# Optimization experiments

Measured on AMD Instinct MI355X. Metric: run time of the kernel, lower is better.

## Reference

```python
import jax, jax.numpy as jnp
import numpy as np

N_NODES = 256  # num_eeg_channels; reshape in head forces node count == channels

def setup_inputs() -> dict:
    key = jax.random.key(0)
    ks = jax.random.split(key, 16)
    T, H, L, E = 30000, 512, 256, 32768
    def w(k, shape):
        return jax.random.normal(k, shape, jnp.float32) / np.sqrt(shape[0]).astype(np.float32)
    return {
        "eeg_nodes": jax.random.normal(ks[0], (N_NODES, T), jnp.float32),
        "eeg_idx": jax.random.randint(ks[1], (2, E), 0, N_NODES),
        "eeg_attr": jax.random.uniform(ks[2], (E,), jnp.float32),
        # struct_featurizer GIN: conv1 MLP [T,H,H], conv2 MLP [H,L,L]
        "Ws1a": w(ks[3], (T, H)), "bs1a": jnp.zeros((H,), jnp.float32),
        "Ws1b": w(ks[4], (H, H)), "bs1b": jnp.zeros((H,), jnp.float32),
        "Ws2a": w(ks[5], (H, L)), "bs2a": jnp.zeros((L,), jnp.float32),
        "Ws2b": w(ks[6], (L, L)), "bs2b": jnp.zeros((L,), jnp.float32),
        # gin_scorer GIN: conv1 MLP [L,H,H], conv2 MLP [H,1,1]
        "Wc1a": w(ks[7], (L, H)), "bc1a": jnp.zeros((H,), jnp.float32),
        "Wc1b": w(ks[8], (H, H)), "bc1b": jnp.zeros((H,), jnp.float32),
        "Wc2a": w(ks[9], (H, 1)), "bc2a": jnp.zeros((1,), jnp.float32),
        "Wc2b": w(ks[10], (1, 1)), "bc2b": jnp.zeros((1,), jnp.float32),
        # dementia head: Linear(N*L, 1)
        "Wd": w(ks[11], (N_NODES * L, 1)), "bd": jnp.zeros((1,), jnp.float32),
    }


def _gin_conv(x, src, dst, W1, b1, W2, b2):
    # GINConv, eps=0: nn(x + sum_{j in N(i)} x_j); edge weights unsupported/ignored.
    agg = jax.ops.segment_sum(x[src], dst, num_segments=N_NODES)
    h = x + agg
    h = jax.nn.relu(h @ W1 + b1)  # MLP([in, out, out]) = Linear-ReLU-Linear
    return h @ W2 + b2


def reference(eeg_nodes, eeg_idx, eeg_attr,
              Ws1a, bs1a, Ws1b, bs1b, Ws2a, bs2a, Ws2b, bs2b,
              Wc1a, bc1a, Wc1b, bc1b, Wc2a, bc2a, Wc2b, bc2b,
              Wd, bd):
    src, dst = eeg_idx[0], eeg_idx[1]
    # struct_featurizer (2-layer GIN; inter-layer ReLU, edge_weight ignored by GINConv)
    h = _gin_conv(eeg_nodes, src, dst, Ws1a, bs1a, Ws1b, bs1b)
    h = jax.nn.relu(h)
    feat = _gin_conv(h, src, dst, Ws2a, bs2a, Ws2b, bs2b)  # [N, L]
    # gin_scorer (2-layer GIN)
    s = _gin_conv(feat, src, dst, Wc1a, bc1a, Wc1b, bc1b)
    s = jax.nn.relu(s)
    s = _gin_conv(s, src, dst, Wc2a, bc2a, Wc2b, bc2b)  # [N, 1]
    region_scores = jax.nn.sigmoid(s)
    flat = feat.reshape(1, -1)  # [1, N*L]
    dementia_pred = jax.nn.sigmoid(flat @ Wd + bd)  # [1, 1]
    return dementia_pred, region_scores
```

## Files before the change

### kernel.cpp

```cpp
#include <hip/hip_runtime.h>
#include <math.h>

#define N_NODES 256
#define T_DIM   30000
#define KP      30016
#define H_DIM   512
#define L_DIM   256

typedef __attribute__((ext_vector_type(8))) short short8;
typedef __attribute__((ext_vector_type(4))) float floatx4;

__device__ __forceinline__ unsigned short f2b(float f) {
    unsigned u = __float_as_uint(f);
    u += 0x7fffu + ((u >> 16) & 1u);
    return (unsigned short)(u >> 16);
}

__device__ __forceinline__ float4 zero4() {
    float4 z; z.x = z.y = z.z = z.w = 0.f; return z;
}

__global__ __launch_bounds__(256)
void k_prep(const float* __restrict__ W, const float* __restrict__ x,
            unsigned short* __restrict__ Wt, unsigned short* __restrict__ xb,
            float* __restrict__ P, float* __restrict__ dem,
            float* __restrict__ u) {
    __shared__ float tile[64][65];
    const int b = blockIdx.x, t = threadIdx.x;
    if (b < 3752) {
        const int k0 = (b % 469) << 6;
        const int c0 = (b / 469) << 6;
        const int rr = t >> 4, c4 = (t & 15) << 2;
        #pragma unroll
        for (int i = 0; i < 4; ++i) {
            const int k = k0 + rr + (i << 4);
            float4 v = (k < T_DIM)
                           ? *(const float4*)&W[(size_t)k * H_DIM + c0 + c4]
                           : zero4();
            tile[rr + (i << 4)][c4 + 0] = v.x;
            tile[rr + (i << 4)][c4 + 1] = v.y;
            tile[rr + (i << 4)][c4 + 2] = v.z;
            tile[rr + (i << 4)][c4 + 3] = v.w;
        }
        __syncthreads();
        const int cr = t >> 4, k4 = (t & 15) << 2;
        #pragma unroll
        for (int i = 0; i < 4; ++i) {
            const int c = cr + (i << 4);
            ushort4 o;
            o.x = f2b(tile[k4 + 0][c]);
            o.y = f2b(tile[k4 + 1][c]);
            o.z = f2b(tile[k4 + 2][c]);
            o.w = f2b(tile[k4 + 3][c]);
            *(ushort4*)&Wt[(size_t)(c0 + c) * KP + k0 + k4] = o;
        }
    } else if (b < 7504) {
        const int e0 = (b - 3752) * 2048 + t * 8;
        const int row = e0 / KP;
        const int col = e0 % KP;
        short8 o;
        if (col < T_DIM) {
            float4 v0 = *(const float4*)&x[(size_t)row * T_DIM + col];
            float4 v1 = *(const float4*)&x[(size_t)row * T_DIM + col + 4];
            o[0] = (short)f2b(v0.x); o[1] = (short)f2b(v0.y);
            o[2] = (short)f2b(v0.z); o[3] = (short)f2b(v0.w);
            o[4] = (short)f2b(v1.x); o[5] = (short)f2b(v1.y);
            o[6] = (short)f2b(v1.z); o[7] = (short)f2b(v1.w);
        } else {
            o = (short8){0, 0, 0, 0, 0, 0, 0, 0};
        }
        *(short8*)&xb[e0] = o;
    } else if (b < 7568) {
        const int i0 = ((b - 7504) << 10) + (t << 2);
        float4 v;
        v.x = ((i0 + 0) >> 8) == ((i0 + 0) & 255) ? 1.f : 0.f;
        v.y = ((i0 + 1) >> 8) == ((i0 + 1) & 255) ? 1.f : 0.f;
        v.z = ((i0 + 2) >> 8) == ((i0 + 2) & 255) ? 1.f : 0.f;
        v.w = ((i0 + 3) >> 8) == ((i0 + 3) & 255) ? 1.f : 0.f;
        *(float4*)&P[i0] = v;
    } else {
        if (t < 256) u[t] = 0.f;
        if (t == 0) *dem = 0.f;
    }
}

__global__ void k_init_P(float* P, float* dem, float* u) {
    int t = blockIdx.x * blockDim.x + threadIdx.x;
    P[t] = ((t >> 8) == (t & 255)) ? 1.0f : 0.0f;
    if (t == 0) *dem = 0.0f;
    if (t < 256) u[t] = 0.0f;
}

__global__ void k_count_edges(const int* __restrict__ idx, int E, float* P) {
    int e = blockIdx.x * blockDim.x + threadIdx.x;
    if (e < E) {
        int s = idx[e];
        int d = idx[E + e];
        atomicAdd(&P[d * N_NODES + s], 1.0f);
    }
}

__global__ void k_zero(float* p, int n) {
    int t = blockIdx.x * blockDim.x + threadIdx.x;
    if (t < n) p[t] = 0.0f;
}

__global__ __launch_bounds__(256)
void k_reduce(const float4* __restrict__ Y1p, float4* __restrict__ Y1, int nz,
              const int* __restrict__ idx, int E, float* __restrict__ P) {
    const int b = blockIdx.x, t = threadIdx.x;
    if (b < 128) {
        const int i = (b << 8) | t;
        float4 s = Y1p[i];
        #pragma unroll 4
        for (int z = 1; z < nz; ++z) {
            float4 v = Y1p[(size_t)z * 32768 + i];
            s.x += v.x; s.y += v.y; s.z += v.z; s.w += v.w;
        }
        Y1[i] = s;
    } else {
        const int e = ((b - 128) << 8) + t;
        if (e < E) {
            int s = idx[e];
            int d = idx[E + e];
            atomicAdd(&P[d * N_NODES + s], 1.0f);
        }
    }
}

__global__ __launch_bounds__(256)
void k_gemm_bf16(const unsigned short* __restrict__ xb,
                 const unsigned short* __restrict__ Wt,
                 float* __restrict__ outp, int kc) {
    __shared__ __align__(16) unsigned short Al[128 * 64];
    __shared__ __align__(16) unsigned short Bl[128 * 64];

    const int t = threadIdx.x;
    const int orig = blockIdx.x;
    const int q = gridDim.x >> 3;
    const int L = (orig & 7) * q + (orig >> 3);
    const int tile = L & 7;
    const int colBase = (tile & 3) << 7;
    const int rowBase = (tile >> 2) << 7;
    const int z = L >> 3;
    const int kb0 = z * kc;
    const int kend = min(kb0 + kc, KP);
    const int nchunk = (kend - kb0) >> 6;

    const int sr = t >> 1, sg = (t & 1) << 2;
    const int br = t >> 3, bhc = t & 7;
    const unsigned short* axp = xb + (size_t)(rowBase + sr) * KP + sg * 8;
    const unsigned short* bwp = Wt + (size_t)(colBase + br) * KP + bhc * 8;

    const int w    = t >> 6;
    const int wr   = (w >> 1) << 6;
    const int wc   = (w & 1) << 6;
    const int lane = t & 63;
    const int lm   = lane & 15;
    const int lq   = (lane >> 4) << 3;

    floatx4 acc[4][4];
    #pragma unroll
    for (int i = 0; i < 4; ++i)
        #pragma unroll
        for (int j = 0; j < 4; ++j)
            acc[i][j] = (floatx4){0.f, 0.f, 0.f, 0.f};

    short8 pa[4], pb[4];

#define GLOAD(C) do {                                                          \
        const int kg_ = kb0 + (C) * 64;                                        \
        _Pragma("unroll")                                                      \
        for (int i_ = 0; i_ < 4; ++i_)                                         \
            pa[i_] = *(const short8*)(axp + kg_ + i_ * 8);                     \
        _Pragma("unroll")                                                      \
        for (int i_ = 0; i_ < 4; ++i_)                                         \
            pb[i_] = *(const short8*)(bwp + (size_t)(32 * i_) * KP + kg_);     \
    } while (0)

    GLOAD(0);

    #pragma unroll 1
    for (int c = 0; c < nchunk; ++c) {
        __syncthreads();
        #pragma unroll
        for (int i = 0; i < 4; ++i) {
            const int ga = (sg + i) ^ (sr & 7);
            *(short8*)&Al[sr * 64 + ga * 8] = pa[i];
        }
        #pragma unroll
        for (int i = 0; i < 4; ++i) {
            const int row = br + 32 * i;
            const int gb  = bhc ^ (row & 7);
            *(short8*)&Bl[row * 64 + gb * 8] = pb[i];
        }
        __syncthreads();

        if (c + 1 < nchunk) GLOAD(c + 1);

        #pragma unroll
        for (int s = 0; s < 2; ++s) {
            const int gbase = (s << 2) | (lq >> 3);
            short8 af[4], bf[4];
            #pragma unroll
            for (int i = 0; i < 4; ++i) {
                const int R = wr + i * 16 + lm;
                af[i] = *(const short8*)&Al[R * 64 + ((gbase ^ (R & 7)) << 3)];
            }
            #pragma unroll
            for (int j = 0; j < 4; ++j) {
                const int Cc = wc + j * 16 + lm;
                bf[j] = *(const short8*)&Bl[Cc * 64 + ((gbase ^ (Cc & 7)) << 3)];
            }
            #pragma unroll
            for (int i = 0; i < 4; ++i)
                #pragma unroll
                for (int j = 0; j < 4; ++j)
                    acc[i][j] = __builtin_amdgcn_mfma_f32_16x16x32_bf16(
                        af[i], bf[j], acc[i][j], 0, 0, 0);
        }
    }
#undef GLOAD

    float* op = outp + (size_t)z * (N_NODES * H_DIM);
    const int rq = (lane >> 4) << 2;
    #pragma unroll
    for (int i = 0; i < 4; ++i) {
        #pragma unroll
        for (int j = 0; j < 4; ++j) {
            const int r  = rowBase + wr + i * 16 + rq;
            const int cc = colBase + wc + j * 16 + lm;
            op[(size_t)(r + 0) * H_DIM + cc] = acc[i][j][0];
            op[(size_t)(r + 1) * H_DIM + cc] = acc[i][j][1];
            op[(size_t)(r + 2) * H_DIM + cc] = acc[i][j][2];
            op[(size_t)(r + 3) * H_DIM + cc] = acc[i][j][3];
        }
    }
}

__global__ __launch_bounds__(256)
void k_gemm_big_atomic(const float* __restrict__ x, const float* __restrict__ W,
                       float* __restrict__ outp, int kc) {
    __shared__ float xs[16 * 140];
    __shared__ float ws[16 * 132];
    const int t  = threadIdx.x;
    const int colBase = blockIdx.x * 128;
    const int rowBase = blockIdx.y * 128;
    const int kb0  = blockIdx.z * kc;
    const int kend = min(kb0 + kc, T_DIM);
    const int nchunk = (kend > kb0) ? ((kend - kb0) >> 4) : 0;
    const int lr  = t >> 2, lkq = (t & 3) * 4;
    const int wkk = t >> 5, wcq = (t & 31) * 4;
    const int tx  = t & 15, ty = t >> 4;
    float acc[8][8];
    #pragma unroll
    for (int i = 0; i < 8; ++i)
        #pragma unroll
        for (int j = 0; j < 8; ++j) acc[i][j] = 0.0f;
    #pragma unroll 1
    for (int c = 0; c < nchunk; ++c) {
        int kb = kb0 + c * 16;
        __syncthreads();
        const float* xp = x + (size_t)(rowBase + lr) * T_DIM + kb + lkq;
        float4 xa = *(const float4*)xp;
        float4 xb4 = *(const float4*)(xp + (size_t)64 * T_DIM);
        const float* wp = W + (size_t)(kb + wkk) * H_DIM + colBase + wcq;
        float4 wa = *(const float4*)wp;
        float4 wb = *(const float4*)(wp + 8 * H_DIM);
        xs[(lkq + 0) * 140 + lr] = xa.x; xs[(lkq + 1) * 140 + lr] = xa.y;
        xs[(lkq + 2) * 140 + lr] = xa.z; xs[(lkq + 3) * 140 + lr] = xa.w;
        xs[(lkq + 0) * 140 + lr + 64] = xb4.x; xs[(lkq + 1) * 140 + lr + 64] = xb4.y;
        xs[(lkq + 2) * 140 + lr + 64] = xb4.z; xs[(lkq + 3) * 140 + lr + 64] = xb4.w;
        *(float4*)&ws[wkk * 132 + wcq]       = wa;
        *(float4*)&ws[(wkk + 8) * 132 + wcq] = wb;
        __syncthreads();
        #pragma unroll
        for (int kk = 0; kk < 16; ++kk) {
            float a[8], b[8];
            *(float4*)&a[0] = *(const float4*)&xs[kk * 140 + ty * 8];
            *(float4*)&a[4] = *(const float4*)&xs[kk * 140 + ty * 8 + 4];
            *(float4*)&b[0] = *(const float4*)&ws[kk * 132 + tx * 8];
            *(float4*)&b[4] = *(const float4*)&ws[kk * 132 + tx * 8 + 4];
            #pragma unroll
            for (int i = 0; i < 8; ++i)
                #pragma unroll
                for (int j = 0; j < 8; ++j)
                    acc[i][j] = fmaf(a[i], b[j], acc[i][j]);
        }
    }
    if (nchunk == 0) return;
    #pragma unroll
    for (int i = 0; i < 8; ++i) {
        int r = rowBase + ty * 8 + i;
        #pragma unroll
        for (int j = 0; j < 8; ++j)
            atomicAdd(&outp[r * H_DIM + colBase + tx * 8 + j], acc[i][j]);
    }
}

template<int K, int N, int MODE>
__global__ __launch_bounds__(64)
void k_mstage(const float* __restrict__ A, const float* __restrict__ B,
              const float* __restrict__ bias, float* __restrict__ out, int act,
              const float* __restrict__ Wd, float* __restrict__ dem,
              const float* __restrict__ uW, float* __restrict__ u) {
    const int lane = threadIdx.x;
    const int wv = blockIdx.x;
    const int nct = N >> 4;
    const int r0 = (wv / nct) << 4;
    const int c0 = (wv % nct) << 4;
    const int lm   = lane & 15;
    const int lq   = (lane >> 4) << 3;

    floatx4 accE = {0.f, 0.f, 0.f, 0.f};
    floatx4 accO = {0.f, 0.f, 0.f, 0.f};
    const float* ap = A + (size_t)(r0 + lm) * K + lq;
    const float* bp = B + (size_t)lq * N + c0 + lm;

    #pragma unroll 2
    for (int kb = 0; kb < K; kb += 64) {
        {
            float4 a0 = *(const float4*)(ap + kb);
            float4 a1 = *(const float4*)(ap + kb + 4);
            const float* bq = bp + (size_t)kb * N;
            float b0 = bq[0],           b1 = bq[(size_t)N];
            float b2 = bq[(size_t)2*N], b3 = bq[(size_t)3*N];
            float b4 = bq[(size_t)4*N], b5 = bq[(size_t)5*N];
            float b6 = bq[(size_t)6*N], b7 = bq[(size_t)7*N];
            short8 af, bf;
            af[0] = (short)f2b(a0.x); af[1] = (short)f2b(a0.y);
            af[2] = (short)f2b(a0.z); af[3] = (short)f2b(a0.w);
            af[4] = (short)f2b(a1.x); af[5] = (short)f2b(a1.y);
            af[6] = (short)f2b(a1.z); af[7] = (short)f2b(a1.w);
            bf[0] = (short)f2b(b0); bf[1] = (short)f2b(b1);
            bf[2] = (short)f2b(b2); bf[3] = (short)f2b(b3);
            bf[4] = (short)f2b(b4); bf[5] = (short)f2b(b5);
            bf[6] = (short)f2b(b6); bf[7] = (short)f2b(b7);
            accE = __builtin_amdgcn_mfma_f32_16x16x32_bf16(af, bf, accE, 0, 0, 0);
        }
        {
            const int k2 = kb + 32;
            float4 a0 = *(const float4*)(ap + k2);
            float4 a1 = *(const float4*)(ap + k2 + 4);
            const float* bq = bp + (size_t)k2 * N;
            float b0 = bq[0],           b1 = bq[(size_t)N];
            float b2 = bq[(size_t)2*N], b3 = bq[(size_t)3*N];
            float b4 = bq[(size_t)4*N], b5 = bq[(size_t)5*N];
            float b6 = bq[(size_t)6*N], b7 = bq[(size_t)7*N];
            short8 af, bf;
            af[0] = (short)f2b(a0.x); af[1] = (short)f2b(a0.y);
            af[2] = (short)f2b(a0.z); af[3] = (short)f2b(a0.w);
            af[4] = (short)f2b(a1.x); af[5] = (short)f2b(a1.y);
            af[6] = (short)f2b(a1.z); af[7] = (short)f2b(a1.w);
            bf[0] = (short)f2b(b0); bf[1] = (short)f2b(b1);
            bf[2] = (short)f2b(b2); bf[3] = (short)f2b(b3);
            bf[4] = (short)f2b(b4); bf[5] = (short)f2b(b5);
            bf[6] = (short)f2b(b6); bf[7] = (short)f2b(b7);
            accO = __builtin_amdgcn_mfma_f32_16x16x32_bf16(af, bf, accO, 0, 0, 0);
        }
    }

    const float bb = bias ? bias[c0 + lm] : 0.f;
    const int rq = (lane >> 4) << 2;
    float v[4];
    #pragma unroll
    for (int i = 0; i < 4; ++i) {
        v[i] = accE[i] + accO[i] + bb;
        if (act) v[i] = fmaxf(v[i], 0.f);
    }

    if (MODE == 2) {
        const float uw = uW[c0 + lm];
        #pragma unroll
        for (int i = 0; i < 4; ++i) {
            float p = v[i] * uw;
            #pragma unroll
            for (int off = 8; off; off >>= 1) p += __shfl_down(p, off, 16);
            if (lm == 0) atomicAdd(&u[r0 + rq + i], p);
        }
        return;
    }
    #pragma unroll
    for (int i = 0; i < 4; ++i)
        out[(size_t)(r0 + rq + i) * N + c0 + lm] = v[i];
    if (MODE == 1) {
        float p = 0.f;
        #pragma unroll
        for (int i = 0; i < 4; ++i)
            p += v[i] * Wd[(r0 + rq + i) * 256 + c0 + lm];
        #pragma unroll
        for (int off = 32; off; off >>= 1) p += __shfl_down(p, off, 64);
        if (lane == 0) atomicAdd(dem, p);
    }
}

__device__ __forceinline__ float sigmoidf(float x) {
    return 1.0f / (1.0f + expf(-x));
}

__global__ __launch_bounds__(256)
void k_final(const float* __restrict__ P, const float* __restrict__ u,
             const float* __restrict__ dem,
             const float* __restrict__ bc2a, const float* __restrict__ Wc2b,
             const float* __restrict__ bc2b, const float* __restrict__ bd,
             float* __restrict__ out) {
    __shared__ float red[4];
    const int b = blockIdx.x, t = threadIdx.x;
    float pv = P[b * 256 + t] * u[t];
    #pragma unroll
    for (int off = 32; off; off >>= 1) pv += __shfl_down(pv, off, 64);
    if ((t & 63) == 0) red[t >> 6] = pv;
    __syncthreads();
    if (t == 0) {
        float v = red[0] + red[1] + red[2] + red[3];
        float h2 = fmaxf(v + bc2a[0], 0.f);
        out[1 + b] = sigmoidf(h2 * Wc2b[0] + bc2b[0]);
        if (b == 0) out[0] = sigmoidf(*dem + bd[0]);
    }
}

extern "C" void kernel_launch(void* const* d_in, const int* in_sizes, int n_in,
                              void* d_out, int out_size, void* d_ws, size_t ws_size,
                              hipStream_t stream) {
    const float* x    = (const float*)d_in[0];
    const int*   idx  = (const int*)d_in[1];
    const float* Ws1a = (const float*)d_in[3];
    const float* bs1a = (const float*)d_in[4];
    const float* Ws1b = (const float*)d_in[5];
    const float* bs1b = (const float*)d_in[6];
    const float* Ws2a = (const float*)d_in[7];
    const float* bs2a = (const float*)d_in[8];
    const float* Ws2b = (const float*)d_in[9];
    const float* bs2b = (const float*)d_in[10];
    const float* Wc1a = (const float*)d_in[11];
    const float* bc1a = (const float*)d_in[12];
    const float* Wc1b = (const float*)d_in[13];
    const float* bc1b = (const float*)d_in[14];
    const float* Wc2a = (const float*)d_in[15];
    const float* bc2a = (const float*)d_in[16];
    const float* Wc2b = (const float*)d_in[17];
    const float* bc2b = (const float*)d_in[18];
    const float* Wd   = (const float*)d_in[19];
    const float* bd   = (const float*)d_in[20];
    float* out = (float*)d_out;
    const int E = in_sizes[1] / 2;

    float* w    = (float*)d_ws;
    float* P    = w;
    float* Y1   = P + 65536;
    float* bufA = Y1 + 131072;
    float* bufB = bufA + 131072;
    float* feat = bufB + 131072;
    float* u    = feat + 65536;
    float* dem  = u + 256;
    float* WtF  = dem + 64;
    const size_t WT_F = ((size_t)H_DIM * KP) / 2;
    float* XbF  = WtF + WT_F;
    const size_t XB_F = ((size_t)N_NODES * KP) / 2;
    float* Y1p  = XbF + XB_F;
    unsigned short* Wt = (unsigned short*)WtF;
    unsigned short* xb = (unsigned short*)XbF;

    const long long fixed = (long long)(Y1p - w);
    const long long avail = (long long)(ws_size / 4) - fixed;
    int maxsplit = (avail > 0) ? (int)(avail / 131072) : 0;
    int nz = 0, kc = 0;
    const int CH64 = 469;
    if (maxsplit >= 2) {
        int splits = maxsplit < 64 ? maxsplit : 64;
        int cps = (CH64 + splits - 1) / splits;
        nz = (CH64 + cps - 1) / cps;
        kc = cps * 64;
    }

    if (nz > 0) {
        k_prep<<<7569, 256, 0, stream>>>(Ws1a, x, Wt, xb, P, dem, u);
        k_gemm_bf16<<<8 * nz, 256, 0, stream>>>(xb, Wt, Y1p, kc);
        k_reduce<<<128 + (E + 255) / 256, 256, 0, stream>>>(
            (const float4*)Y1p, (float4*)Y1, nz, idx, E, P);
    } else {
        k_init_P<<<256, 256, 0, stream>>>(P, dem, u);
        k_count_edges<<<(E + 255) / 256, 256, 0, stream>>>(idx, E, P);
        k_zero<<<512, 256, 0, stream>>>(Y1, N_NODES * H_DIM);
        k_gemm_big_atomic<<<dim3(4, 2, 63), 256, 0, stream>>>(x, Ws1a, Y1, 480);
    }

    k_mstage<256, 512, 0><<<512, 64, 0, stream>>>(P,    Y1,   bs1a, bufA, 1, 0, 0, 0, 0);
    k_mstage<512, 512, 0><<<512, 64, 0, stream>>>(bufA, Ws1b, bs1b, bufB, 1, 0, 0, 0, 0);
    k_mstage<256, 512, 0><<<512, 64, 0, stream>>>(P,    bufB, 0,    bufA, 0, 0, 0, 0, 0);
    k_mstage<512, 256, 0><<<256, 64, 0, stream>>>(bufA, Ws2a, bs2a, bufB, 1, 0, 0, 0, 0);
    k_mstage<256, 256, 1><<<256, 64, 0, stream>>>(bufB, Ws2b, bs2b, feat, 0, Wd, dem, 0, 0);
    k_mstage<256, 256, 0><<<256, 64, 0, stream>>>(P,    feat, 0,    bufA, 0, 0, 0, 0, 0);
    k_mstage<256, 512, 0><<<512, 64, 0, stream>>>(bufA, Wc1a, bc1a, bufB, 1, 0, 0, 0, 0);
    k_mstage<512, 512, 2><<<512, 64, 0, stream>>>(bufB, Wc1b, bc1b, 0,    1, 0, 0, Wc2a, u);
    k_final<<<256, 256, 0, stream>>>(P, u, dem, bc2a, Wc2b, bc2b, bd, out);
}
```

Baseline: 228.1 us.

## Load MFMA fragments directly from global memory, dropping LDS staging

After: 243.2 us. 1.07x slower.

```diff
diff --git a/kernel.cpp b/kernel.cpp
--- a/kernel.cpp
+++ b/kernel.cpp
@@ -132,9 +132,6 @@
 void k_gemm_bf16(const unsigned short* __restrict__ xb,
                  const unsigned short* __restrict__ Wt,
                  float* __restrict__ outp, int kc) {
-    __shared__ __align__(16) unsigned short Al[128 * 64];
-    __shared__ __align__(16) unsigned short Bl[128 * 64];
-
     const int t = threadIdx.x;
     const int orig = blockIdx.x;
     const int q = gridDim.x >> 3;
@@ -147,11 +144,6 @@
     const int kend = min(kb0 + kc, KP);
     const int nchunk = (kend - kb0) >> 6;
 
-    const int sr = t >> 1, sg = (t & 1) << 2;
-    const int br = t >> 3, bhc = t & 7;
-    const unsigned short* axp = xb + (size_t)(rowBase + sr) * KP + sg * 8;
-    const unsigned short* bwp = Wt + (size_t)(colBase + br) * KP + bhc * 8;
-
     const int w    = t >> 6;
     const int wr   = (w >> 1) << 6;
     const int wc   = (w & 1) << 6;
@@ -159,6 +151,9 @@
     const int lm   = lane & 15;
     const int lq   = (lane >> 4) << 3;
 
+    const unsigned short* ap0 = xb + (size_t)(rowBase + wr + lm) * KP + lq;
+    const unsigned short* bp0 = Wt + (size_t)(colBase + wc + lm) * KP + lq;
+
     floatx4 acc[4][4];
     #pragma unroll
     for (int i = 0; i < 4; ++i)
@@ -166,61 +161,38 @@
         for (int j = 0; j < 4; ++j)
             acc[i][j] = (floatx4){0.f, 0.f, 0.f, 0.f};
 
-    short8 pa[4], pb[4];
-
-#define GLOAD(C) do {                                                          \
-        const int kg_ = kb0 + (C) * 64;                                        \
+    short8 aE[4], bE[4], aO[4], bO[4];
+
+#define LDF(SA, SB, KO) do {                                                   \
         _Pragma("unroll")                                                      \
         for (int i_ = 0; i_ < 4; ++i_)                                         \
-            pa[i_] = *(const short8*)(axp + kg_ + i_ * 8);                     \
+            SA[i_] = *(const short8*)(ap0 + (size_t)(i_ * 16) * KP + (KO));    \
         _Pragma("unroll")                                                      \
-        for (int i_ = 0; i_ < 4; ++i_)                                         \
-            pb[i_] = *(const short8*)(bwp + (size_t)(32 * i_) * KP + kg_);     \
+        for (int j_ = 0; j_ < 4; ++j_)                                         \
+            SB[j_] = *(const short8*)(bp0 + (size_t)(j_ * 16) * KP + (KO));    \
     } while (0)
 
-    GLOAD(0);
+    LDF(aE, bE, kb0);
 
     #pragma unroll 1
     for (int c = 0; c < nchunk; ++c) {
-        __syncthreads();
-        #pragma unroll
-        for (int i = 0; i < 4; ++i) {
-            const int ga = (sg + i) ^ (sr & 7);
-            *(short8*)&Al[sr * 64 + ga * 8] = pa[i];
-        }
-        #pragma unroll
-        for (int i = 0; i < 4; ++i) {
-            const int row = br + 32 * i;
-            const int gb  = bhc ^ (row & 7);
-            *(short8*)&Bl[row * 64 + gb * 8] = pb[i];
-        }
-        __syncthreads();
-
-        if (c + 1 < nchunk) GLOAD(c + 1);
-
-        #pragma unroll
-        for (int s = 0; s < 2; ++s) {
-            const int gbase = (s << 2) | (lq >> 3);
-            short8 af[4], bf[4];
+        const int kb = kb0 + c * 64;
+        LDF(aO, bO, kb + 32);
+        #pragma unroll
+        for (int i = 0; i < 4; ++i)
             #pragma unroll
-            for (int i = 0; i < 4; ++i) {
-                const int R = wr + i * 16 + lm;
-                af[i] = *(const short8*)&Al[R * 64 + ((gbase ^ (R & 7)) << 3)];
-            }
+            for (int j = 0; j < 4; ++j)
+                acc[i][j] = __builtin_amdgcn_mfma_f32_16x16x32_bf16(
+                    aE[i], bE[j], acc[i][j], 0, 0, 0);
+        if (c + 1 < nchunk) LDF(aE, bE, kb + 64);
+        #pragma unroll
+        for (int i = 0; i < 4; ++i)
             #pragma unroll
-            for (int j = 0; j < 4; ++j) {
-                const int Cc = wc + j * 16 + lm;
-                bf[j] = *(const short8*)&Bl[Cc * 64 + ((gbase ^ (Cc & 7)) << 3)];
-            }
-            #pragma unroll
-            for (int i = 0; i < 4; ++i)
-                #pragma unroll
-                for (int j = 0; j < 4; ++j)
-                    acc[i][j] = __builtin_amdgcn_mfma_f32_16x16x32_bf16(
-                        af[i], bf[j], acc[i][j], 0, 0, 0);
-        }
-    }
-#undef GLOAD
+            for (int j = 0; j < 4; ++j)
+                acc[i][j] = __builtin_amdgcn_mfma_f32_16x16x32_bf16(
+                    aO[i], bO[j], acc[i][j], 0, 0, 0);
+    }
+#undef LDF
 
     float* op = outp + (size_t)z * (N_NODES * H_DIM);
     const int rq = (lane >> 4) << 2;
```
